# Kernel optimization log

Measured on AMD Instinct MI355X. Metric: run time of the kernel, lower is better.

## Reference

```python
import jax, jax.numpy as jnp
import numpy as np

TRIANGLE_TABLE = jnp.array([
    [-1,-1,-1,-1,-1,-1],[1,0,2,-1,-1,-1],[4,0,3,-1,-1,-1],[1,4,2,1,3,4],
    [3,1,5,-1,-1,-1],[2,3,0,2,5,3],[1,4,0,1,5,4],[4,2,5,-1,-1,-1],
    [4,5,2,-1,-1,-1],[4,1,0,4,5,1],[3,2,0,3,5,2],[1,3,5,-1,-1,-1],
    [4,1,2,4,3,1],[3,0,4,-1,-1,-1],[2,0,1,-1,-1,-1],[-1,-1,-1,-1,-1,-1]], dtype=jnp.int32)
NUM_TRI_TABLE = jnp.array([0,1,1,2,1,2,2,1,1,2,2,1,2,1,1,0], dtype=jnp.int32)
BASE_TET_EDGES = jnp.array([0,1,0,2,0,3,1,2,1,3,2,3], dtype=jnp.int32)
N_VERTS, N_TETS = 200_000, 1_000_000


def setup_inputs() -> dict:
    key = jax.random.key(0)
    k1, k2, k3 = jax.random.split(key, 3)
    pos_nx3 = jax.random.normal(k1, (N_VERTS, 3), jnp.float32)
    sdf_n = jax.random.normal(k2, (N_VERTS,), jnp.float32)
    tet_fx4 = jax.random.randint(k3, (N_TETS, 4), 0, N_VERTS, dtype=jnp.int32)
    return {"pos_nx3": pos_nx3, "sdf_n": sdf_n, "tet_fx4": tet_fx4}


def _mt_indices(sdf_n, tet_fx4):
    # Index-only part (torch.no_grad in the original). Dynamic shapes -> eager jax.
    occ_n = sdf_n > 0                              # [N]
    occ_fx4 = occ_n[tet_fx4]                       # [T,4]
    occ_sum = occ_fx4.sum(-1)
    valid = (occ_sum > 0) & (occ_sum < 4)          # surface-crossing tets
    tets_v = tet_fx4[valid]                        # [Tv,4]
    occ_v = occ_fx4[valid]
    # 6 edges per tet, sorted so (min,max) -> dedup identical to torch sort_edges+unique
    all_edges = jnp.sort(tets_v[:, BASE_TET_EDGES].reshape(-1, 2), axis=1)  # [Tv*6,2]
    unique_edges, idx_map = jnp.unique(all_edges, axis=0, return_inverse=True)
    idx_map = idx_map.reshape(-1)
    mask_edges = occ_n[unique_edges].sum(-1) == 1  # exactly one endpoint inside
    # compacting map: -1 for non-crossing edges, running index for crossing ones
    mapping = jnp.where(mask_edges, jnp.cumsum(mask_edges.astype(jnp.int32)) - 1, -1)
    idx_map = mapping[idx_map].reshape(-1, 6)      # [Tv,6] per-tet edge->vertex ids
    interp_v = unique_edges[mask_edges]            # [Ne,2] endpoint indices
    return valid, occ_v, idx_map, interp_v


def _interp_verts(pos, sdf, interp_v):
    e_pos = pos[interp_v]                                   # [Ne,2,3]
    e_sdf = sdf[interp_v] * jnp.array([1.0, -1.0], sdf.dtype)  # [s0,-s1]
    denom = e_sdf.sum(1, keepdims=True)                     # s0 - s1
    w = e_sdf[:, ::-1] / denom                              # [-s1, s0] / (s0-s1)
    return (e_pos * w[..., None]).sum(1)                    # [Ne,3]


def _map_uv(face_gidx, max_idx):
    Ngrid = int(np.ceil(np.sqrt((max_idx + 1) // 2)))
    lin = jnp.linspace(0.0, 1.0 - 1.0 / Ngrid, Ngrid, dtype=jnp.float32)
    tex_y, tex_x = jnp.meshgrid(lin, lin, indexing='ij')
    pad = 0.9 / Ngrid
    uvs = jnp.stack([tex_x, tex_y, tex_x + pad, tex_y,
                     tex_x + pad, tex_y + pad, tex_x, tex_y + pad], axis=-1).reshape(-1, 2)
    tet_raw = face_gidx // 2
    tet_idx = (tet_raw // Ngrid) * Ngrid + tet_raw % Ngrid
    tri_idx = face_gidx % 2
    uv_idx = jnp.stack([tet_idx * 4, tet_idx * 4 + tri_idx + 1,
                        tet_idx * 4 + tri_idx + 2], axis=-1).reshape(-1, 3)
    return uvs, uv_idx


def reference(pos_nx3, sdf_n, tet_fx4):
    valid, occ_v, idx_map, interp_v = _mt_indices(sdf_n, tet_fx4)
    verts = _interp_verts(pos_nx3, sdf_n, interp_v)
    # triangle-table lookup
    v_id = jnp.array([1, 2, 4, 8], jnp.int32)
    tetindex = (occ_v.astype(jnp.int32) * v_id).sum(-1)     # [Tv]
    num_tri = NUM_TRI_TABLE[tetindex]
    m1, m2 = num_tri == 1, num_tri == 2
    faces1 = jnp.take_along_axis(idx_map[m1], TRIANGLE_TABLE[tetindex[m1]][:, :3], axis=1).reshape(-1, 3)
    faces2 = jnp.take_along_axis(idx_map[m2], TRIANGLE_TABLE[tetindex[m2]][:, :6], axis=1).reshape(-1, 3)
    faces = jnp.concatenate([faces1, faces2], axis=0)
    tet_gidx = jnp.nonzero(valid)[0].astype(jnp.int32)
    face_gidx = jnp.concatenate([
        tet_gidx[m1] * 2,
        jnp.stack([tet_gidx[m2] * 2, tet_gidx[m2] * 2 + 1], axis=-1).reshape(-1)], axis=0)
    uvs, uv_idx = _map_uv(face_gidx, tet_fx4.shape[0] * 2)
    return verts, faces, uvs, uv_idx
```

## Files before the change

### kernel.cpp

```cpp
#include <hip/hip_runtime.h>
#include <cmath>

typedef unsigned long long u64;
typedef unsigned int u32;
typedef unsigned char u8;

#define SCAN_BLOCK 256
#define SCAN_ELEMS 8
#define SCAN_TILE (SCAN_BLOCK * SCAN_ELEMS)

#define BIN_SHIFT 9
#define BIN_VR 512
#define TETS_PER_BLOCK 2048

__constant__ int d_NUMTRI[16] = {0,1,1,2,1,2,2,1,1,2,2,1,2,1,1,0};
__constant__ int d_TRI[16][6] = {
 {-1,-1,-1,-1,-1,-1},{1,0,2,-1,-1,-1},{4,0,3,-1,-1,-1},{1,4,2,1,3,4},
 {3,1,5,-1,-1,-1},{2,3,0,2,5,3},{1,4,0,1,5,4},{4,2,5,-1,-1,-1},
 {4,5,2,-1,-1,-1},{4,1,0,4,5,1},{3,2,0,3,5,2},{1,3,5,-1,-1,-1},
 {4,1,2,4,3,1},{3,0,4,-1,-1,-1},{2,0,1,-1,-1,-1},{-1,-1,-1,-1,-1,-1}};
__constant__ int d_E0[6] = {0,0,0,1,1,2};
__constant__ int d_E1[6] = {1,2,3,2,3,3};

template <typename T>
__global__ void scanA_t(const T* in, T* out, int n, T* blockSums) {
    __shared__ T tsum[SCAN_BLOCK];
    int tbase = blockIdx.x * SCAN_TILE + threadIdx.x * SCAN_ELEMS;
    T vals[SCAN_ELEMS];
    T run = 0;
    for (int k = 0; k < SCAN_ELEMS; ++k) {
        int i = tbase + k;
        T v = (i < n) ? in[i] : (T)0;
        vals[k] = run;
        run += v;
    }
    tsum[threadIdx.x] = run;
    __syncthreads();
    for (int off = 1; off < SCAN_BLOCK; off <<= 1) {
        T v = (threadIdx.x >= (unsigned)off) ? tsum[threadIdx.x - off] : (T)0;
        __syncthreads();
        tsum[threadIdx.x] += v;
        __syncthreads();
    }
    T texcl = (threadIdx.x == 0) ? (T)0 : tsum[threadIdx.x - 1];
    for (int k = 0; k < SCAN_ELEMS; ++k) {
        int i = tbase + k;
        if (i < n) out[i] = texcl + vals[k];
    }
    if (threadIdx.x == SCAN_BLOCK - 1) blockSums[blockIdx.x] = tsum[SCAN_BLOCK - 1];
}

template <typename T>
__global__ void scanCf_t(T* out, int n, const T* bs, int nb, T* totalOut) {
    __shared__ T sh[2048];
    for (int i = threadIdx.x; i < 2048; i += 256) sh[i] = (i < nb) ? bs[i] : (T)0;
    __syncthreads();
    for (int off = 1; off < 2048; off <<= 1) {
        T v[8];
        for (int k = 0; k < 8; ++k) {
            int i = threadIdx.x + k * 256;
            v[k] = (i >= off) ? sh[i - off] : (T)0;
        }
        __syncthreads();
        for (int k = 0; k < 8; ++k) sh[threadIdx.x + k * 256] += v[k];
        __syncthreads();
    }
    if (totalOut && blockIdx.x == 0 && threadIdx.x == 0)
        *totalOut = (nb > 0) ? sh[nb - 1] : (T)0;
    T add = (blockIdx.x == 0) ? (T)0 : sh[blockIdx.x - 1];
    int base = blockIdx.x * SCAN_TILE;
    int end = base + SCAN_TILE; if (end > n) end = n;
    for (int i = base + threadIdx.x; i < end; i += SCAN_BLOCK) out[i] += add;
}

__global__ void k_scanA_dual(const u64* in64, u64* out64, int n64, u64* bs64,
                             const u32* in32, u32* out32, int n32, u32* bs32,
                             int nbT) {
    __shared__ u64 tsum[SCAN_BLOCK];
    if ((int)blockIdx.x < nbT) {
        int tbase = blockIdx.x * SCAN_TILE + threadIdx.x * SCAN_ELEMS;
        u64 vals[SCAN_ELEMS]; u64 run = 0;
        for (int k = 0; k < SCAN_ELEMS; ++k) {
            int i = tbase + k;
            u64 v = (i < n64) ? in64[i] : 0ull;
            vals[k] = run; run += v;
        }
        tsum[threadIdx.x] = run;
        __syncthreads();
        for (int off = 1; off < SCAN_BLOCK; off <<= 1) {
            u64 v = (threadIdx.x >= (unsigned)off) ? tsum[threadIdx.x - off] : 0ull;
            __syncthreads();
            tsum[threadIdx.x] += v;
            __syncthreads();
        }
        u64 texcl = (threadIdx.x == 0) ? 0ull : tsum[threadIdx.x - 1];
        for (int k = 0; k < SCAN_ELEMS; ++k) {
            int i = tbase + k;
            if (i < n64) out64[i] = texcl + vals[k];
        }
        if (threadIdx.x == SCAN_BLOCK - 1) bs64[blockIdx.x] = tsum[SCAN_BLOCK - 1];
    } else {
        int blk = (int)blockIdx.x - nbT;
        int tbase = blk * SCAN_TILE + threadIdx.x * SCAN_ELEMS;
        u32 vals[SCAN_ELEMS]; u32 run = 0;
        for (int k = 0; k < SCAN_ELEMS; ++k) {
            int i = tbase + k;
            u32 v = (i < n32) ? in32[i] : 0u;
            vals[k] = run; run += v;
        }
        tsum[threadIdx.x] = (u64)run;
        __syncthreads();
        for (int off = 1; off < SCAN_BLOCK; off <<= 1) {
            u64 v = (threadIdx.x >= (unsigned)off) ? tsum[threadIdx.x - off] : 0ull;
            __syncthreads();
            tsum[threadIdx.x] += v;
            __syncthreads();
        }
        u32 texcl = (threadIdx.x == 0) ? 0u : (u32)tsum[threadIdx.x - 1];
        for (int k = 0; k < SCAN_ELEMS; ++k) {
            int i = tbase + k;
            if (i < n32) out32[i] = texcl + vals[k];
        }
        if (threadIdx.x == SCAN_BLOCK - 1) bs32[blk] = (u32)tsum[SCAN_BLOCK - 1];
    }
}

__global__ void k_scanCf_dual(u64* out64, int n64, const u64* bs64, int nb64,
                              u64* total64,
                              u32* out32, int n32, const u32* bs32, int nb32,
                              u32* total32, int nbT) {
    __shared__ u64 sh[2048];
    if ((int)blockIdx.x < nbT) {
        for (int i = threadIdx.x; i < 2048; i += 256)
            sh[i] = (i < nb64) ? bs64[i] : 0ull;
        __syncthreads();
        for (int off = 1; off < 2048; off <<= 1) {
            u64 v[8];
            for (int k = 0; k < 8; ++k) {
                int i = threadIdx.x + k * 256;
                v[k] = (i >= off) ? sh[i - off] : 0ull;
            }
            __syncthreads();
            for (int k = 0; k < 8; ++k) sh[threadIdx.x + k * 256] += v[k];
            __syncthreads();
        }
        if (total64 && blockIdx.x == 0 && threadIdx.x == 0)
            *total64 = (nb64 > 0) ? sh[nb64 - 1] : 0ull;
        u64 add = (blockIdx.x == 0) ? 0ull : sh[blockIdx.x - 1];
        int base = blockIdx.x * SCAN_TILE;
        int end = base + SCAN_TILE; if (end > n64) end = n64;
        for (int i = base + threadIdx.x; i < end; i += SCAN_BLOCK) out64[i] += add;
    } else {
        int blk = (int)blockIdx.x - nbT;
        for (int i = threadIdx.x; i < 2048; i += 256)
            sh[i] = (i < nb32) ? (u64)bs32[i] : 0ull;
        __syncthreads();
        for (int off = 1; off < 2048; off <<= 1) {
            u64 v[8];
            for (int k = 0; k < 8; ++k) {
                int i = threadIdx.x + k * 256;
                v[k] = (i >= off) ? sh[i - off] : 0ull;
            }
            __syncthreads();
            for (int k = 0; k < 8; ++k) sh[threadIdx.x + k * 256] += v[k];
            __syncthreads();
        }
        if (total32 && blk == 0 && threadIdx.x == 0)
            *total32 = (nb32 > 0) ? (u32)sh[nb32 - 1] : 0u;
        u32 add = (blk == 0) ? 0u : (u32)sh[blk - 1];
        int base = blk * SCAN_TILE;
        int end = base + SCAN_TILE; if (end > n32) end = n32;
        for (int i = base + threadIdx.x; i < end; i += SCAN_BLOCK) out32[i] += add;
    }
}

__global__ __launch_bounds__(256) void k_classify_hist(
    const int* tet, const float* sdf, u8* ti8, u64* tetPack,
    u32* blockHist, u32* bigCnt, int T, int NB, int gB) {
    if (blockIdx.x == 0 && threadIdx.x == 0) *bigCnt = 0;
    __shared__ u32 hist[BIN_VR];
    for (int i = threadIdx.x; i < NB; i += 256) hist[i] = 0;
    __syncthreads();
    int base = blockIdx.x * TETS_PER_BLOCK;
    for (int it = 0; it < TETS_PER_BLOCK / 256; ++it) {
        int t = base + it * 256 + threadIdx.x;
        if (t < T) {
            int4 q = reinterpret_cast<const int4*>(tet)[t];
            int ti = (sdf[q.x] > 0.0f ? 1 : 0) | (sdf[q.y] > 0.0f ? 2 : 0) |
                     (sdf[q.z] > 0.0f ? 4 : 0) | (sdf[q.w] > 0.0f ? 8 : 0);
            ti8[t] = (u8)ti;
            int nt = d_NUMTRI[ti];
            tetPack[t] = ((u64)(nt == 1 ? 1 : 0) << 21) | (u64)(nt == 2 ? 1 : 0);
            if (nt != 0) {
                int idx[4] = {q.x, q.y, q.z, q.w};
                #pragma unroll
                for (int e = 0; e < 6; ++e) {
                    int e0 = d_E0[e], e1 = d_E1[e];
                    if (((ti >> e0) ^ (ti >> e1)) & 1) {
                        int a = idx[e0], b = idx[e1];
                        int mn = a < b ? a : b;
                        atomicAdd(&hist[mn >> BIN_SHIFT], 1u);
                    }
                }
            }
        }
    }
    __syncthreads();
    for (int i = threadIdx.x; i < NB; i += 256)
        blockHist[(size_t)i * gB + blockIdx.x] = hist[i];
}

__global__ __launch_bounds__(256) void k_binfill(
    const int* tet, const u8* ti8, const u32* blockHistScan,
    u64* binRec, int T, int NB, int gB) {
    __shared__ u32 cur[BIN_VR];
    for (int i = threadIdx.x; i < NB; i += 256)
        cur[i] = blockHistScan[(size_t)i * gB + blockIdx.x];
    __syncthreads();
    int base = blockIdx.x * TETS_PER_BLOCK;
    for (int it = 0; it < TETS_PER_BLOCK / 256; ++it) {
        int t = base + it * 256 + threadIdx.x;
        if (t < T) {
            int ti = ti8[t];
            if (d_NUMTRI[ti] != 0) {
                int4 q = reinterpret_cast<const int4*>(tet)[t];
                int idx[4] = {q.x, q.y, q.z, q.w};
                #pragma unroll
                for (int e = 0; e < 6; ++e) {
                    int e0 = d_E0[e], e1 = d_E1[e];
                    if (((ti >> e0) ^ (ti >> e1)) & 1) {
                        int a = idx[e0], b = idx[e1];
                        int mn = a < b ? a : b;
                        int mx = a < b ? b : a;
                        u32 slot = atomicAdd(&cur[mn >> BIN_SHIFT], 1u);
                        u32 rec = ((u32)(mn & (BIN_VR - 1)) << 18) | (u32)mx;
                        u32 pv = 6u * (u32)t + (u32)e;
                        binRec[slot] = ((u64)pv << 32) | (u64)rec;
                    }
                }
            }
        }
    }
}

__global__ __launch_bounds__(256) void k_binsort(
    const u32* blockHistScan, const u32* totalPtr, const u64* binRec,
    u32* bucketCnt, u32* bucketStart, uint2* rec2, int V, int NB, int gB) {
    int bin = blockIdx.x;
    __shared__ u32 hist[BIN_VR];
    __shared__ u32 sc[BIN_VR];
    __shared__ u32 cur[BIN_VR];
    for (int i = threadIdx.x; i < BIN_VR; i += 256) hist[i] = 0;
    __syncthreads();
    u32 s = blockHistScan[(size_t)bin * gB];
    u32 e = (bin + 1 < NB) ? blockHistScan[(size_t)(bin + 1) * gB] : *totalPtr;
    for (u32 i = s + threadIdx.x; i < e; i += 256)
        atomicAdd(&hist[((u32)binRec[i]) >> 18], 1u);
    __syncthreads();
    int t0 = threadIdx.x, t1 = threadIdx.x + 256;
    sc[t0] = hist[t0];
    sc[t1] = hist[t1];
    __syncthreads();
    for (int off = 1; off < BIN_VR; off <<= 1) {
        u32 v0 = (t0 >= off) ? sc[t0 - off] : 0u;
        u32 v1 = (t1 >= off) ? sc[t1 - off] : 0u;
        __syncthreads();
        sc[t0] += v0; sc[t1] += v1;
        __syncthreads();
    }
    int vbase = bin << BIN_SHIFT;
    for (int i = threadIdx.x; i < BIN_VR; i += 256) {
        int v = vbase + i;
        u32 h = hist[i];
        u32 abs0 = s + sc[i] - h;
        if (v < V) {
            bucketCnt[v] = h;
            bucketStart[v] = abs0;
        }
        cur[i] = abs0;
    }
    __syncthreads();
    for (u32 i = s + threadIdx.x; i < e; i += 256) {
        u64 r = binRec[i];
        u32 rec = (u32)r;
        u32 pv = (u32)(r >> 32);
        u32 slot = atomicAdd(&cur[rec >> 18], 1u);
        rec2[slot] = make_uint2(rec & 0x3FFFFu, pv);
    }
}

__global__ __launch_bounds__(256) void k_sortdedup(
    const u32* bucketCnt, const u32* bucketStart, uint2* rec2,
    u8* idxmap, u32* crossCnt, u32* bigList, u32* bigCnt, int V)
{
    int v = blockIdx.x * 4 + (threadIdx.x >> 6);
    if (v >= V) return;
    int lane = threadIdx.x & 63;
    int n = (int)bucketCnt[v];
    if (n == 0) { if (lane == 0) crossCnt[v] = 0; return; }
    if (n > 64) {
        if (lane == 0) bigList[atomicAdd(bigCnt, 1u)] = (u32)v;
        return;
    }
    long long start = (long long)bucketStart[v];
    uint2 rp = (lane < n) ? rec2[start + lane] : make_uint2(0xFFFFFFFFu, 0u);
    u32 key = rp.x, prov = rp.y;
    int rank = 0;
    for (int j = 0; j < n; ++j) {
        u32 kj = (u32)__shfl((int)key, j);
        rank += (kj < key || (kj == key && j < lane)) ? 1 : 0;
    }
    u32 sorted = (u32)__builtin_amdgcn_ds_permute(rank << 2, (int)key);
    u32 prev = (u32)__shfl((int)sorted, lane - 1);
    bool nf = (lane < n) && (lane == 0 || prev != sorted);
    u64 m = __ballot(nf);
    int idx = __popcll(m & ((1ull << lane) - 1ull));
    if (nf) rec2[start + idx].x = sorted;
    int ldSorted = nf ? idx : idx - 1;
    int ldOrig = __shfl(ldSorted, rank);
    if (lane < n) idxmap[prov] = (u8)ldOrig;
    if (lane == 0) crossCnt[v] = (u32)__popcll(m);
}

__global__ __launch_bounds__(256) void k_sortbig(
    const u32* bigList, const u32* bigCnt, const u32* bucketCnt,
    const u32* bucketStart, uint2* rec2, u8* idxmap, u32* crossCnt)
{
    int nbig = (int)*bigCnt;
    int lane = threadIdx.x & 63;
    int wave = (blockIdx.x << 2) + (threadIdx.x >> 6);
    int stride = gridDim.x << 2;
    for (int b = wave; b < nbig; b += stride) {
        int v = (int)bigList[b];
        int n = (int)bucketCnt[v];
        long long start = (long long)bucketStart[v];
        if (n <= 256) {
            int chunks = (n + 63) >> 6;
            u32 key[4], prov[4], kf[4];
            int myi[4];
            #pragma unroll
            for (int c = 0; c < 4; ++c) {
                myi[c] = (c << 6) + lane;
                key[c] = 0xFFFFFFFFu; prov[c] = 0u;
                if (c < chunks && myi[c] < n) {
                    uint2 rp = rec2[start + myi[c]];
                    key[c] = rp.x; prov[c] = rp.y;
                }
            }
            bool tie[4] = {false, false, false, false};
            #pragma unroll
            for (int c2 = 0; c2 < 4; ++c2) {
                if (c2 < chunks) {
                    int base2 = c2 << 6;
                    int lim = n - base2; if (lim > 64) lim = 64;
                    for (int j = 0; j < lim; ++j) {
                        u32 kj = (u32)__shfl((int)key[c2], j);
                        int jg = base2 + j;
                        #pragma unroll
                        for (int c = 0; c < 4; ++c) {
                            if (c < chunks)
                                tie[c] = tie[c] | (kj == key[c] && jg < myi[c]);
                        }
                    }
                }
            }
            u32 uq = 0;
            #pragma unroll
            for (int c = 0; c < 4; ++c) {
                bool isf = (c < chunks) && (myi[c] < n) && !tie[c];
                kf[c] = key[c] | (isf ? 0x80000000u : 0u);
                u64 bal = __ballot(isf);
                uq += (u32)__popcll(bal);
            }
            int uless[4] = {0, 0, 0, 0};
            #pragma unroll
            for (int c2 = 0; c2 < 4; ++c2) {
                if (c2 < chunks) {
                    int base2 = c2 << 6;
                    int lim = n - base2; if (lim > 64) lim = 64;
                    for (int j = 0; j < lim; ++j) {
                        u32 kfj = (u32)__shfl((int)kf[c2], j);
                        u32 kj = kfj & 0x7FFFFFFFu;
                        bool fj = (kfj & 0x80000000u) != 0u;
                        #pragma unroll
                        for (int c = 0; c < 4; ++c) {
                            if (c < chunks)
                                uless[c] += (fj && kj < key[c]) ? 1 : 0;
                        }
                    }
                }
            }
            #pragma unroll
            for (int c = 0; c < 4; ++c) {
                if (c < chunks && myi[c] < n) {
                    if (kf[c] & 0x80000000u)
                        rec2[start + uless[c]].x = key[c];
                    idxmap[prov[c]] = (u8)uless[c];
                }
            }
            if (lane == 0) crossCnt[v] = uq;
        } else if (lane == 0) {
            for (int i = 1; i < n; ++i) {
                uint2 kk = rec2[start + i];
                int j = i - 1;
                while (j >= 0 && rec2[start + j].x > kk.x) {
                    rec2[start + j + 1] = rec2[start + j]; --j;
                }
                rec2[start + j + 1] = kk;
            }
            int uc = 0; u32 prev = 0xFFFFFFFFu;
            for (int i = 0; i < n; ++i) {
                uint2 r = rec2[start + i];
                if (r.x != prev) { rec2[start + uc].x = r.x; ++uc; prev = r.x; }
                idxmap[r.y] = (u8)(uc - 1);
            }
            crossCnt[v] = (u32)uc;
        }
    }
}

__global__ __launch_bounds__(256) void k_verts(
    const u32* crossCnt, const u32* bucketStart, const uint2* rec2, const u32* crossScan,
    const float* pos, const float* sdf, float* out, int V)
{
    int v = blockIdx.x * 8 + (threadIdx.x >> 5);
    if (v >= V) return;
    int slane = threadIdx.x & 31;
    int u = (int)crossCnt[v];
    if (u == 0) return;
    long long start = (long long)bucketStart[v];
    int cBase = (int)crossScan[v];
    float s0 = sdf[v];
    float p0x = pos[3 * v], p0y = pos[3 * v + 1], p0z = pos[3 * v + 2];
    for (int i = slane; i < u; i += 32) {
        int b = (int)rec2[start + i].x;
        long long k = cBase + i;
        float s1 = sdf[b];
        float d = s0 - s1;
        float w0 = -s1 / d, w1 = s0 / d;
        out[3 * k + 0] = p0x * w0 + pos[3 * b + 0] * w1;
        out[3 * k + 1] = p0y * w0 + pos[3 * b + 1] * w1;
        out[3 * k + 2] = p0z * w0 + pos[3 * b + 2] * w1;
    }
}

__global__ void k_faces(const int* tet, const u8* ti8, const u64* tetScan,
                        const u8* idxmap, const u32* crossScan,
                        const u64* meta0, const u32* NePtr,
                        float* out, int T, int Ngrid, long long uvFloats)
{
    int t = blockIdx.x * 256 + threadIdx.x;
    int uvTotal = Ngrid * Ngrid;
    if (t >= T && t >= uvTotal) return;

    u64 tot = *meta0;
    int C1 = (int)((tot >> 21) & 0x1fffffull);
    int C2 = (int)(tot & 0x1fffffull);
    int Ne = (int)*NePtr;
    long long facesBase = 3LL * Ne;
    long long F = (long long)C1 + 2LL * C2;
    long long uvBase = facesBase + 3LL * F;
    long long uvIdxBase = uvBase + uvFloats;

    if (t < uvTotal) {
        int i = t / Ngrid, j = t % Ngrid;
        double step = (Ngrid > 1) ? (1.0 - 1.0 / (double)Ngrid) / (double)(Ngrid - 1) : 0.0;
        float x = (float)((double)j * step);
        float y = (float)((double)i * step);
        float pad = (float)(0.9 / (double)Ngrid);
        long long o = uvBase + 8LL * t;
        out[o + 0] = x;       out[o + 1] = y;
        out[o + 2] = x + pad; out[o + 3] = y;
        out[o + 4] = x + pad; out[o + 5] = y + pad;
        out[o + 6] = x;       out[o + 7] = y + pad;
    }
    if (t >= T) return;

    int ti = ti8[t];
    int nt = d_NUMTRI[ti];
    if (nt == 0) return;

    int4 q = reinterpret_cast<const int4*>(tet)[t];
    int idx[4] = {q.x, q.y, q.z, q.w};
    const unsigned short* imp =
        reinterpret_cast<const unsigned short*>(idxmap + 6ll * t);
    unsigned short w0 = imp[0], w1 = imp[1], w2 = imp[2];
    u32 im[6] = {(u32)(w0 & 0xFF), (u32)(w0 >> 8),
                 (u32)(w1 & 0xFF), (u32)(w1 >> 8),
                 (u32)(w2 & 0xFF), (u32)(w2 >> 8)};
    const int* row = d_TRI[ti];

    int emap[6];
    unsigned done = 0;
    float fv[6];
    #pragma unroll
    for (int j = 0; j < 6; ++j) {
        if (j >= 3 * nt) break;
        int e = row[j];
        if (!((done >> e) & 1)) {
            done |= 1u << e;
            int a = idx[d_E0[e]], b = idx[d_E1[e]];
            if (b < a) a = b;
            emap[e] = (int)crossScan[a] + (int)im[e];
        }
        fv[j] = (float)emap[e];
    }

    u64 sc = tetScan[t];
    int r1s = (int)((sc >> 21) & 0x1fffffull);
    int r2s = (int)(sc & 0x1fffffull);
    int tet_idx = (t / Ngrid) * Ngrid + (t % Ngrid);

    if (nt == 1) {
        long long f = r1s;
        out[facesBase + 3 * f + 0] = fv[0];
        out[facesBase + 3 * f + 1] = fv[1];
        out[facesBase + 3 * f + 2] = fv[2];
        out[uvIdxBase + 3 * f + 0] = (float)(4 * tet_idx);
        out[uvIdxBase + 3 * f + 1] = (float)(4 * tet_idx + 1);
        out[uvIdxBase + 3 * f + 2] = (float)(4 * tet_idx + 2);
    } else {
        long long f0 = (long long)C1 + 2LL * r2s;
        out[facesBase + 3 * f0 + 0] = fv[0];
        out[facesBase + 3 * f0 + 1] = fv[1];
        out[facesBase + 3 * f0 + 2] = fv[2];
        out[facesBase + 3 * (f0 + 1) + 0] = fv[3];
        out[facesBase + 3 * (f0 + 1) + 1] = fv[4];
        out[facesBase + 3 * (f0 + 1) + 2] = fv[5];
        out[uvIdxBase + 3 * f0 + 0] = (float)(4 * tet_idx);
        out[uvIdxBase + 3 * f0 + 1] = (float)(4 * tet_idx + 1);
        out[uvIdxBase + 3 * f0 + 2] = (float)(4 * tet_idx + 2);
        out[uvIdxBase + 3 * (f0 + 1) + 0] = (float)(4 * tet_idx);
        out[uvIdxBase + 3 * (f0 + 1) + 1] = (float)(4 * tet_idx + 2);
        out[uvIdxBase + 3 * (f0 + 1) + 2] = (float)(4 * tet_idx + 3);
    }
}

template <typename T>
static void run_scan2(const T* in, T* out, int n, T* blockSums, T* totalOut,
                      hipStream_t stream) {
    int nb = (n + SCAN_TILE - 1) / SCAN_TILE;
    scanA_t<T><<<nb, SCAN_BLOCK, 0, stream>>>(in, out, n, blockSums);
    scanCf_t<T><<<nb, SCAN_BLOCK, 0, stream>>>(out, n, blockSums, nb, totalOut);
}

extern "C" void kernel_launch(void* const* d_in, const int* in_sizes, int n_in,
                              void* d_out, int out_size, void* d_ws, size_t ws_size,
                              hipStream_t stream) {
    const float* pos = (const float*)d_in[0];
    const float* sdf = (const float*)d_in[1];
    const int* tet = (const int*)d_in[2];
    int V = in_sizes[1];
    int T = in_sizes[2] / 4;
    float* out = (float*)d_out;

    int NB = (V + BIN_VR - 1) / BIN_VR;
    int gB = (T + TETS_PER_BLOCK - 1) / TETS_PER_BLOCK;
    int nHist = NB * gB;

    char* p = (char*)d_ws;
    auto alloc = [&](size_t bytes) -> void* {
        void* r = (void*)p;
        p += (bytes + 255) & ~(size_t)255;
        return r;
    };
    u8*  ti8           = (u8*) alloc((size_t)T);
    u64* tetPack       = (u64*)alloc((size_t)T * 8);
    u64* tetScan       = (u64*)alloc((size_t)T * 8);
    u32* blockHist     = (u32*)alloc((size_t)nHist * 4);
    u32* blockHistScan = (u32*)alloc((size_t)nHist * 4);
    u64* binRec        = (u64*)alloc((size_t)6 * T * 8);
    u32* bucketCnt     = (u32*)alloc((size_t)V * 4);
    u32* bucketStart   = (u32*)alloc((size_t)V * 4);
    u32* crossCnt      = (u32*)alloc((size_t)V * 4);
    u32* crossScan     = (u32*)alloc((size_t)V * 4);
    uint2* rec2        = (uint2*)alloc(((size_t)6 * T + 4 * (size_t)V) * 8);
    u32* bigList       = (u32*)alloc((size_t)V * 4);
    u64* blockSums64   = (u64*)alloc(2048 * 8);
    u32* blockSums32   = (u32*)alloc(2048 * 4);
    u64* meta64        = (u64*)alloc(8 * 8);
    u32* NePtr         = (u32*)(meta64 + 4);
    u32* NeInstPtr     = (u32*)(meta64 + 5);
    u32* bigCnt        = (u32*)(meta64 + 6);

    u8* idxmap = (u8*)binRec;

    long long M = (2LL * T + 1) / 2;
    int Ngrid = (int)std::sqrt((double)M);
    while ((long long)Ngrid * Ngrid < M) ++Ngrid;
    if (Ngrid < 1) Ngrid = 1;
    long long uvFloats = 8LL * Ngrid * Ngrid;

    int gV4 = (V + 3) / 4;
    int gV8 = (V + 7) / 8;
    long long fw = (long long)Ngrid * Ngrid;
    if (fw < (long long)T) fw = T;
    int gFU = (int)((fw + 255) / 256);

    int nbT = (T + SCAN_TILE - 1) / SCAN_TILE;
    int nbH = (nHist + SCAN_TILE - 1) / SCAN_TILE;

    k_classify_hist<<<gB, 256, 0, stream>>>(tet, sdf, ti8, tetPack, blockHist,
                                            bigCnt, T, NB, gB);
    k_scanA_dual<<<nbT + nbH, SCAN_BLOCK, 0, stream>>>(
        tetPack, tetScan, T, blockSums64,
        blockHist, blockHistScan, nHist, blockSums32, nbT);
    k_scanCf_dual<<<nbT + nbH, SCAN_BLOCK, 0, stream>>>(
        tetScan, T, blockSums64, nbT, meta64,
        blockHistScan, nHist, blockSums32, nbH, NeInstPtr, nbT);
    k_binfill<<<gB, 256, 0, stream>>>(tet, ti8, blockHistScan, binRec,
                                      T, NB, gB);
    k_binsort<<<NB, 256, 0, stream>>>(blockHistScan, NeInstPtr, binRec,
                                      bucketCnt, bucketStart, rec2, V, NB, gB);
    k_sortdedup<<<gV4, 256, 0, stream>>>(bucketCnt, bucketStart, rec2,
                                         idxmap, crossCnt, bigList, bigCnt, V);
    k_sortbig<<<1024, 256, 0, stream>>>(bigList, bigCnt, bucketCnt, bucketStart,
                                        rec2, idxmap, crossCnt);
    run_scan2<u32>(crossCnt, crossScan, V, blockSums32, NePtr, stream);
    k_verts<<<gV8, 256, 0, stream>>>(crossCnt, bucketStart, rec2, crossScan,
                                     pos, sdf, out, V);
    k_faces<<<gFU, 256, 0, stream>>>(tet, ti8, tetScan, idxmap, crossScan,
                                     meta64, NePtr, out, T, Ngrid, uvFloats);
}
```

Before: 411.0 us.

## Fuse big-bucket sort into dedup and merge crossing-count scan with vertex interpolation

Buckets with more than 64 records are now handled inline in the dedup kernel instead of being deferred to a separate big-bucket kernel through an atomic list. The dedup kernel also adds each bucket's crossing count into per-256-vertex tile sums with atomics. A new kernel scans those tile sums, does an in-block scan of the per-vertex counts and writes the interpolated vertices, replacing two scan launches plus the separate vertex kernel. This cuts three kernel launches, but the vertex write now uses one thread per vertex with a serial loop instead of 32 lanes, and the rare large buckets can stall a whole wave inside the dedup kernel.

```diff
diff --git a/kernel.cpp b/kernel.cpp
--- a/kernel.cpp
+++ b/kernel.cpp
@@ -12,6 +12,7 @@
 #define BIN_SHIFT 9
 #define BIN_VR 512
 #define TETS_PER_BLOCK 2048
+#define VT_SHIFT 8
 
 __constant__ int d_NUMTRI[16] = {0,1,1,2,1,2,2,1,1,2,2,1,2,1,1,0};
 __constant__ int d_TRI[16][6] = {
@@ -22,56 +23,6 @@
 __constant__ int d_E0[6] = {0,0,0,1,1,2};
 __constant__ int d_E1[6] = {1,2,3,2,3,3};
 
-template <typename T>
-__global__ void scanA_t(const T* in, T* out, int n, T* blockSums) {
-    __shared__ T tsum[SCAN_BLOCK];
-    int tbase = blockIdx.x * SCAN_TILE + threadIdx.x * SCAN_ELEMS;
-    T vals[SCAN_ELEMS];
-    T run = 0;
-    for (int k = 0; k < SCAN_ELEMS; ++k) {
-        int i = tbase + k;
-        T v = (i < n) ? in[i] : (T)0;
-        vals[k] = run;
-        run += v;
-    }
-    tsum[threadIdx.x] = run;
-    __syncthreads();
-    for (int off = 1; off < SCAN_BLOCK; off <<= 1) {
-        T v = (threadIdx.x >= (unsigned)off) ? tsum[threadIdx.x - off] : (T)0;
-        __syncthreads();
-        tsum[threadIdx.x] += v;
-        __syncthreads();
-    }
-    T texcl = (threadIdx.x == 0) ? (T)0 : tsum[threadIdx.x - 1];
-    for (int k = 0; k < SCAN_ELEMS; ++k) {
-        int i = tbase + k;
-        if (i < n) out[i] = texcl + vals[k];
-    }
-    if (threadIdx.x == SCAN_BLOCK - 1) blockSums[blockIdx.x] = tsum[SCAN_BLOCK - 1];
-}
-
-template <typename T>
-__global__ void scanCf_t(T* out, int n, const T* bs, int nb, T* totalOut) {
-    __shared__ T sh[2048];
-    for (int i = threadIdx.x; i < 2048; i += 256) sh[i] = (i < nb) ? bs[i] : (T)0;
-    __syncthreads();
-    for (int off = 1; off < 2048; off <<= 1) {
-        T v[8];
-        for (int k = 0; k < 8; ++k) {
-            int i = threadIdx.x + k * 256;
-            v[k] = (i >= off) ? sh[i - off] : (T)0;
-        }
-        __syncthreads();
-        for (int k = 0; k < 8; ++k) sh[threadIdx.x + k * 256] += v[k];
-        __syncthreads();
-    }
-    if (totalOut && blockIdx.x == 0 && threadIdx.x == 0)
-        *totalOut = (nb > 0) ? sh[nb - 1] : (T)0;
-    T add = (blockIdx.x == 0) ? (T)0 : sh[blockIdx.x - 1];
-    int base = blockIdx.x * SCAN_TILE;
-    int end = base + SCAN_TILE; if (end > n) end = n;
-    for (int i = base + threadIdx.x; i < end; i += SCAN_BLOCK) out[i] += add;
-}
 
 __global__ void k_scanA_dual(const u64* in64, u64* out64, int n64, u64* bs64,
                              const u32* in32, u32* out32, int n32, u32* bs32,
@@ -176,8 +127,9 @@
 
 __global__ __launch_bounds__(256) void k_classify_hist(
     const int* tet, const float* sdf, u8* ti8, u64* tetPack,
-    u32* blockHist, u32* bigCnt, int T, int NB, int gB) {
-    if (blockIdx.x == 0 && threadIdx.x == 0) *bigCnt = 0;
+    u32* blockHist, u32* tileSum, int nTiles, int T, int NB, int gB) {
+    if (blockIdx.x == 0)
+        for (int i = threadIdx.x; i < nTiles; i += 256) tileSum[i] = 0u;
     __shared__ u32 hist[BIN_VR];
     for (int i = threadIdx.x; i < NB; i += 256) hist[i] = 0;
     __syncthreads();
@@ -291,115 +243,100 @@
 
 __global__ __launch_bounds__(256) void k_sortdedup(
     const u32* bucketCnt, const u32* bucketStart, uint2* rec2,
-    u8* idxmap, u32* crossCnt, u32* bigList, u32* bigCnt, int V)
+    u8* idxmap, u32* crossCnt, u32* tileSum, int V)
 {
     int v = blockIdx.x * 4 + (threadIdx.x >> 6);
     if (v >= V) return;
     int lane = threadIdx.x & 63;
     int n = (int)bucketCnt[v];
     if (n == 0) { if (lane == 0) crossCnt[v] = 0; return; }
-    if (n > 64) {
-        if (lane == 0) bigList[atomicAdd(bigCnt, 1u)] = (u32)v;
-        return;
-    }
     long long start = (long long)bucketStart[v];
-    uint2 rp = (lane < n) ? rec2[start + lane] : make_uint2(0xFFFFFFFFu, 0u);
-    u32 key = rp.x, prov = rp.y;
-    int rank = 0;
-    for (int j = 0; j < n; ++j) {
-        u32 kj = (u32)__shfl((int)key, j);
-        rank += (kj < key || (kj == key && j < lane)) ? 1 : 0;
-    }
-    u32 sorted = (u32)__builtin_amdgcn_ds_permute(rank << 2, (int)key);
-    u32 prev = (u32)__shfl((int)sorted, lane - 1);
-    bool nf = (lane < n) && (lane == 0 || prev != sorted);
-    u64 m = __ballot(nf);
-    int idx = __popcll(m & ((1ull << lane) - 1ull));
-    if (nf) rec2[start + idx].x = sorted;
-    int ldSorted = nf ? idx : idx - 1;
-    int ldOrig = __shfl(ldSorted, rank);
-    if (lane < n) idxmap[prov] = (u8)ldOrig;
-    if (lane == 0) crossCnt[v] = (u32)__popcll(m);
-}
-
-__global__ __launch_bounds__(256) void k_sortbig(
-    const u32* bigList, const u32* bigCnt, const u32* bucketCnt,
-    const u32* bucketStart, uint2* rec2, u8* idxmap, u32* crossCnt)
-{
-    int nbig = (int)*bigCnt;
-    int lane = threadIdx.x & 63;
-    int wave = (blockIdx.x << 2) + (threadIdx.x >> 6);
-    int stride = gridDim.x << 2;
-    for (int b = wave; b < nbig; b += stride) {
-        int v = (int)bigList[b];
-        int n = (int)bucketCnt[v];
-        long long start = (long long)bucketStart[v];
-        if (n <= 256) {
-            int chunks = (n + 63) >> 6;
-            u32 key[4], prov[4], kf[4];
-            int myi[4];
-            #pragma unroll
-            for (int c = 0; c < 4; ++c) {
-                myi[c] = (c << 6) + lane;
-                key[c] = 0xFFFFFFFFu; prov[c] = 0u;
-                if (c < chunks && myi[c] < n) {
-                    uint2 rp = rec2[start + myi[c]];
-                    key[c] = rp.x; prov[c] = rp.y;
-                }
-            }
-            bool tie[4] = {false, false, false, false};
-            #pragma unroll
-            for (int c2 = 0; c2 < 4; ++c2) {
-                if (c2 < chunks) {
-                    int base2 = c2 << 6;
-                    int lim = n - base2; if (lim > 64) lim = 64;
-                    for (int j = 0; j < lim; ++j) {
-                        u32 kj = (u32)__shfl((int)key[c2], j);
-                        int jg = base2 + j;
-                        #pragma unroll
-                        for (int c = 0; c < 4; ++c) {
-                            if (c < chunks)
-                                tie[c] = tie[c] | (kj == key[c] && jg < myi[c]);
-                        }
+    u32 u = 0;
+
+    if (n <= 64) {
+        uint2 rp = (lane < n) ? rec2[start + lane] : make_uint2(0xFFFFFFFFu, 0u);
+        u32 key = rp.x, prov = rp.y;
+        int rank = 0;
+        for (int j = 0; j < n; ++j) {
+            u32 kj = (u32)__shfl((int)key, j);
+            rank += (kj < key || (kj == key && j < lane)) ? 1 : 0;
+        }
+        u32 sorted = (u32)__builtin_amdgcn_ds_permute(rank << 2, (int)key);
+        u32 prev = (u32)__shfl((int)sorted, lane - 1);
+        bool nf = (lane < n) && (lane == 0 || prev != sorted);
+        u64 m = __ballot(nf);
+        int idx = __popcll(m & ((1ull << lane) - 1ull));
+        if (nf) rec2[start + idx].x = sorted;
+        int ldSorted = nf ? idx : idx - 1;
+        int ldOrig = __shfl(ldSorted, rank);
+        if (lane < n) idxmap[prov] = (u8)ldOrig;
+        u = (u32)__popcll(m);
+    } else if (n <= 256) {
+        int chunks = (n + 63) >> 6;
+        u32 key[4], prov[4], kf[4];
+        int myi[4];
+        #pragma unroll
+        for (int c = 0; c < 4; ++c) {
+            myi[c] = (c << 6) + lane;
+            key[c] = 0xFFFFFFFFu; prov[c] = 0u;
+            if (c < chunks && myi[c] < n) {
+                uint2 rp = rec2[start + myi[c]];
+                key[c] = rp.x; prov[c] = rp.y;
+            }
+        }
+        bool tie[4] = {false, false, false, false};
+        #pragma unroll
+        for (int c2 = 0; c2 < 4; ++c2) {
+            if (c2 < chunks) {
+                int base2 = c2 << 6;
+                int lim = n - base2; if (lim > 64) lim = 64;
+                for (int j = 0; j < lim; ++j) {
+                    u32 kj = (u32)__shfl((int)key[c2], j);
+                    int jg = base2 + j;
+                    #pragma unroll
+                    for (int c = 0; c < 4; ++c) {
+                        if (c < chunks)
+                            tie[c] = tie[c] | (kj == key[c] && jg < myi[c]);
                     }
                 }
             }
-            u32 uq = 0;
-            #pragma unroll
-            for (int c = 0; c < 4; ++c) {
-                bool isf = (c < chunks) && (myi[c] < n) && !tie[c];
-                kf[c] = key[c] | (isf ? 0x80000000u : 0u);
-                u64 bal = __ballot(isf);
-                uq += (u32)__popcll(bal);
-            }
-            int uless[4] = {0, 0, 0, 0};
-            #pragma unroll
-            for (int c2 = 0; c2 < 4; ++c2) {
-                if (c2 < chunks) {
-                    int base2 = c2 << 6;
-                    int lim = n - base2; if (lim > 64) lim = 64;
-                    for (int j = 0; j < lim; ++j) {
-                        u32 kfj = (u32)__shfl((int)kf[c2], j);
-                        u32 kj = kfj & 0x7FFFFFFFu;
-                        bool fj = (kfj & 0x80000000u) != 0u;
-                        #pragma unroll
-                        for (int c = 0; c < 4; ++c) {
-                            if (c < chunks)
-                                uless[c] += (fj && kj < key[c]) ? 1 : 0;
-                        }
+        }
+        #pragma unroll
+        for (int c = 0; c < 4; ++c) {
+            bool isf = (c < chunks) && (myi[c] < n) && !tie[c];
+            kf[c] = key[c] | (isf ? 0x80000000u : 0u);
+            u64 bal = __ballot(isf);
+            u += (u32)__popcll(bal);
+        }
+        int uless[4] = {0, 0, 0, 0};
+        #pragma unroll
+        for (int c2 = 0; c2 < 4; ++c2) {
+            if (c2 < chunks) {
+                int base2 = c2 << 6;
+                int lim = n - base2; if (lim > 64) lim = 64;
+                for (int j = 0; j < lim; ++j) {
+                    u32 kfj = (u32)__shfl((int)kf[c2], j);
+                    u32 kj = kfj & 0x7FFFFFFFu;
+                    bool fj = (kfj & 0x80000000u) != 0u;
+                    #pragma unroll
+                    for (int c = 0; c < 4; ++c) {
+                        if (c < chunks)
+                            uless[c] += (fj && kj < key[c]) ? 1 : 0;
                     }
                 }
             }
-            #pragma unroll
-            for (int c = 0; c < 4; ++c) {
-                if (c < chunks && myi[c] < n) {
-                    if (kf[c] & 0x80000000u)
-                        rec2[start + uless[c]].x = key[c];
-                    idxmap[prov[c]] = (u8)uless[c];
-                }
-            }
-            if (lane == 0) crossCnt[v] = uq;
-        } else if (lane == 0) {
+        }
+        #pragma unroll
+        for (int c = 0; c < 4; ++c) {
+            if (c < chunks && myi[c] < n) {
+                if (kf[c] & 0x80000000u)
+                    rec2[start + uless[c]].x = key[c] & 0x7FFFFFFFu;
+                idxmap[prov[c]] = (u8)uless[c];
+            }
+        }
+    } else {
+        int uc = 0;
+        if (lane == 0) {
             for (int i = 1; i < n; ++i) {
                 uint2 kk = rec2[start + i];
                 int j = i - 1;
@@ -408,39 +345,78 @@
                 }
                 rec2[start + j + 1] = kk;
             }
-            int uc = 0; u32 prev = 0xFFFFFFFFu;
+            u32 prev = 0xFFFFFFFFu;
             for (int i = 0; i < n; ++i) {
                 uint2 r = rec2[start + i];
                 if (r.x != prev) { rec2[start + uc].x = r.x; ++uc; prev = r.x; }
                 idxmap[r.y] = (u8)(uc - 1);
             }
-            crossCnt[v] = (u32)uc;
-        }
-    }
-}
-
-__global__ __launch_bounds__(256) void k_verts(
-    const u32* crossCnt, const u32* bucketStart, const uint2* rec2, const u32* crossScan,
+        }
+        u = (u32)__shfl(uc, 0);
+    }
+
+    if (lane == 0) {
+        crossCnt[v] = u;
+        if (u) atomicAdd(&tileSum[v >> VT_SHIFT], u);
+    }
+}
+
+__global__ __launch_bounds__(256) void k_scanverts(
+    const u32* crossCnt, const u32* tileSum, int nTiles,
+    const u32* bucketStart, const uint2* rec2,
+    u32* crossScan, u32* NePtr,
     const float* pos, const float* sdf, float* out, int V)
 {
-    int v = blockIdx.x * 8 + (threadIdx.x >> 5);
-    if (v >= V) return;
-    int slane = threadIdx.x & 31;
-    int u = (int)crossCnt[v];
-    if (u == 0) return;
-    long long start = (long long)bucketStart[v];
-    int cBase = (int)crossScan[v];
-    float s0 = sdf[v];
-    float p0x = pos[3 * v], p0y = pos[3 * v + 1], p0z = pos[3 * v + 2];
-    for (int i = slane; i < u; i += 32) {
-        int b = (int)rec2[start + i].x;
-        long long k = cBase + i;
-        float s1 = sdf[b];
-        float d = s0 - s1;
-        float w0 = -s1 / d, w1 = s0 / d;
-        out[3 * k + 0] = p0x * w0 + pos[3 * b + 0] * w1;
-        out[3 * k + 1] = p0y * w0 + pos[3 * b + 1] * w1;
-        out[3 * k + 2] = p0z * w0 + pos[3 * b + 2] * w1;
+    __shared__ u32 ts[1024];
+    __shared__ u32 sc[256];
+    for (int i = threadIdx.x; i < 1024; i += 256)
+        ts[i] = (i < nTiles) ? tileSum[i] : 0u;
+    __syncthreads();
+    for (int off = 1; off < 1024; off <<= 1) {
+        u32 v0[4];
+        #pragma unroll
+        for (int k = 0; k < 4; ++k) {
+            int i = threadIdx.x + k * 256;
+            v0[k] = (i >= off) ? ts[i - off] : 0u;
+        }
+        __syncthreads();
+        #pragma unroll
+        for (int k = 0; k < 4; ++k) ts[threadIdx.x + k * 256] += v0[k];
+        __syncthreads();
+    }
+    if (blockIdx.x == 0 && threadIdx.x == 0)
+        *NePtr = (nTiles > 0) ? ts[nTiles - 1] : 0u;
+    int tile = blockIdx.x;
+    u32 texcl = (tile == 0) ? 0u : ts[tile - 1];
+
+    int v = (tile << VT_SHIFT) + threadIdx.x;
+    u32 c = (v < V) ? crossCnt[v] : 0u;
+    sc[threadIdx.x] = c;
+    __syncthreads();
+    for (int off = 1; off < 256; off <<= 1) {
+        u32 x = ((int)threadIdx.x >= off) ? sc[threadIdx.x - off] : 0u;
+        __syncthreads();
+        sc[threadIdx.x] += x;
+        __syncthreads();
+    }
+    u32 excl = texcl + sc[threadIdx.x] - c;
+    if (v < V) {
+        crossScan[v] = excl;
+        if (c) {
+            long long start = (long long)bucketStart[v];
+            float s0 = sdf[v];
+            float p0x = pos[3 * v], p0y = pos[3 * v + 1], p0z = pos[3 * v + 2];
+            for (u32 i = 0; i < c; ++i) {
+                int b = (int)rec2[start + i].x;
+                float s1 = sdf[b];
+                float d = s0 - s1;
+                float w0 = -s1 / d, w1 = s0 / d;
+                long long k = (long long)excl + i;
+                out[3 * k + 0] = p0x * w0 + pos[3 * b + 0] * w1;
+                out[3 * k + 1] = p0y * w0 + pos[3 * b + 1] * w1;
+                out[3 * k + 2] = p0z * w0 + pos[3 * b + 2] * w1;
+            }
+        }
     }
 }
 
@@ -536,14 +512,6 @@
     }
 }
 
-template <typename T>
-static void run_scan2(const T* in, T* out, int n, T* blockSums, T* totalOut,
-                      hipStream_t stream) {
-    int nb = (n + SCAN_TILE - 1) / SCAN_TILE;
-    scanA_t<T><<<nb, SCAN_BLOCK, 0, stream>>>(in, out, n, blockSums);
-    scanCf_t<T><<<nb, SCAN_BLOCK, 0, stream>>>(out, n, blockSums, nb, totalOut);
-}
-
 extern "C" void kernel_launch(void* const* d_in, const int* in_sizes, int n_in,
                               void* d_out, int out_size, void* d_ws, size_t ws_size,
                               hipStream_t stream) {
@@ -557,6 +525,7 @@
     int NB = (V + BIN_VR - 1) / BIN_VR;
     int gB = (T + TETS_PER_BLOCK - 1) / TETS_PER_BLOCK;
     int nHist = NB * gB;
+    int nTiles = (V + (1 << VT_SHIFT) - 1) >> VT_SHIFT;
 
     char* p = (char*)d_ws;
     auto alloc = [&](size_t bytes) -> void* {
@@ -575,13 +544,12 @@
     u32* crossCnt      = (u32*)alloc((size_t)V * 4);
     u32* crossScan     = (u32*)alloc((size_t)V * 4);
     uint2* rec2        = (uint2*)alloc(((size_t)6 * T + 4 * (size_t)V) * 8);
-    u32* bigList       = (u32*)alloc((size_t)V * 4);
+    u32* tileSum       = (u32*)alloc(1024 * 4);
     u64* blockSums64   = (u64*)alloc(2048 * 8);
     u32* blockSums32   = (u32*)alloc(2048 * 4);
     u64* meta64        = (u64*)alloc(8 * 8);
     u32* NePtr         = (u32*)(meta64 + 4);
     u32* NeInstPtr     = (u32*)(meta64 + 5);
-    u32* bigCnt        = (u32*)(meta64 + 6);
 
     u8* idxmap = (u8*)binRec;
 
@@ -592,7 +560,6 @@
     long long uvFloats = 8LL * Ngrid * Ngrid;
 
     int gV4 = (V + 3) / 4;
-    int gV8 = (V + 7) / 8;
     long long fw = (long long)Ngrid * Ngrid;
     if (fw < (long long)T) fw = T;
     int gFU = (int)((fw + 255) / 256);
@@ -601,7 +568,7 @@
     int nbH = (nHist + SCAN_TILE - 1) / SCAN_TILE;
 
     k_classify_hist<<<gB, 256, 0, stream>>>(tet, sdf, ti8, tetPack, blockHist,
-                                            bigCnt, T, NB, gB);
+                                            tileSum, nTiles, T, NB, gB);
     k_scanA_dual<<<nbT + nbH, SCAN_BLOCK, 0, stream>>>(
         tetPack, tetScan, T, blockSums64,
         blockHist, blockHistScan, nHist, blockSums32, nbT);
@@ -613,12 +580,10 @@
     k_binsort<<<NB, 256, 0, stream>>>(blockHistScan, NeInstPtr, binRec,
                                       bucketCnt, bucketStart, rec2, V, NB, gB);
     k_sortdedup<<<gV4, 256, 0, stream>>>(bucketCnt, bucketStart, rec2,
-                                         idxmap, crossCnt, bigList, bigCnt, V);
-    k_sortbig<<<1024, 256, 0, stream>>>(bigList, bigCnt, bucketCnt, bucketStart,
-                                        rec2, idxmap, crossCnt);
-    run_scan2<u32>(crossCnt, crossScan, V, blockSums32, NePtr, stream);
-    k_verts<<<gV8, 256, 0, stream>>>(crossCnt, bucketStart, rec2, crossScan,
-                                     pos, sdf, out, V);
+                                         idxmap, crossCnt, tileSum, V);
+    k_scanverts<<<nTiles, 256, 0, stream>>>(crossCnt, tileSum, nTiles,
+                                            bucketStart, rec2, crossScan,
+                                            NePtr, pos, sdf, out, V);
     k_faces<<<gFU, 256, 0, stream>>>(tet, ti8, tetScan, idxmap, crossScan,
                                      meta64, NePtr, out, T, Ngrid, uvFloats);
 }
```

Measured after the change: 785.9 us. 91.2% more time.
